# Kernel tuning notes

Measured on AMD Instinct MI355X. Metric: run time of the kernel, lower is better.

The kernel has to match this reference:

```python
import jax, jax.numpy as jnp
import numpy as np

B, T, D = 4, 4096, 1024
H, KP = 16, 256  # heads, low-rank seq projection dim
DK = D // H


def setup_inputs() -> dict:
    key = jax.random.key(0)
    ks = jax.random.split(key, 8)
    s = 1.0 / np.sqrt(D)
    xav = np.sqrt(6.0 / (T + KP))  # xavier_uniform for (max_seq_len, k_proj_dim)
    return {
        "x": jax.random.normal(ks[0], (B, T, D), jnp.float32),
        "Wq": jax.random.normal(ks[1], (D, D), jnp.float32) * s,
        "Wk": jax.random.normal(ks[2], (D, D), jnp.float32) * s,
        "Wv": jax.random.normal(ks[3], (D, D), jnp.float32) * s,
        "Ek": jax.random.uniform(ks[4], (T, KP), jnp.float32, -xav, xav),
        "Ev": jax.random.uniform(ks[5], (T, KP), jnp.float32, -xav, xav),
        "Wo": jax.random.normal(ks[6], (D, D), jnp.float32) * s,
        "bo": jnp.zeros((D,), jnp.float32),
    }


def reference(x, Wq, Wk, Wv, Ek, Ev, Wo, bo):
    Bx, Tx, _ = x.shape
    # QKV projections -> (B, H, T, DK)
    def split_heads(y):
        return y.reshape(Bx, Tx, H, DK).transpose(0, 2, 1, 3)
    Q = split_heads(x @ Wq)
    K = split_heads(x @ Wk)
    V = split_heads(x @ Wv)
    # Low-rank projection along sequence length: T -> KP
    K_proj = jnp.einsum('bhtd,tk->bhkd', K, Ek[:Tx])
    V_proj = jnp.einsum('bhtd,tk->bhkd', V, Ev[:Tx])
    scale = 1.0 / np.sqrt(DK)
    scores = jnp.einsum('bhtd,bhkd->bhtk', Q, K_proj) * scale
    attn = jax.nn.softmax(scores, axis=-1)
    ctx = jnp.einsum('bhtk,bhkd->bhtd', attn, V_proj)
    out = ctx.transpose(0, 2, 1, 3).reshape(Bx, Tx, D)
    return out @ Wo + bo  # dropout p=0.0 (eval) -> identity
```

## Files before the change

### kernel.cpp

```cpp
#include <hip/hip_runtime.h>

typedef unsigned short u16;
typedef __attribute__((ext_vector_type(8))) short short8;
typedef __attribute__((ext_vector_type(4))) float f32x4;

#define T_SEQ 4096
#define DMODEL 1024
#define NH 16
#define DKH 64
#define KPROJ 256

__device__ __forceinline__ u16 f2bf(float f) {
  union { float f; unsigned u; } v; v.f = f;
  unsigned r = v.u + 0x7FFFu + ((v.u >> 16) & 1u);
  return (u16)(r >> 16);
}
__device__ __forceinline__ float bf2f(u16 h) {
  union { unsigned u; float f; } v; v.u = ((unsigned)h) << 16; return v.f;
}
__device__ __forceinline__ unsigned cvt_pk_bf16(float a, float b) {
  unsigned r;
  asm("v_cvt_pk_bf16_f32 %0, %1, %2" : "=v"(r) : "v"(a), "v"(b));
  return r;
}

__device__ __forceinline__ void gl2lds16(const u16* g, u16* l) {
  __builtin_amdgcn_global_load_lds(
      (const __attribute__((address_space(1))) unsigned int*)g,
      (__attribute__((address_space(3))) unsigned int*)(unsigned int)(unsigned long long)l,
      16, 0, 0);
}

__global__ void sniff_dtype(const u16* __restrict__ x, int* __restrict__ flag) {
  int c = 0;
  for (int i = threadIdx.x; i < 8192; i += 64)
    if ((x[2 * i] & 0x7F80) == 0x7F80) c++;
#pragma unroll
  for (int m = 1; m < 64; m <<= 1) c += __shfl_xor(c, m);
  if (threadIdx.x == 0) *flag = (c > 0) ? 1 : 0;
}

__global__ void transpose_x(const void* __restrict__ in, u16* __restrict__ outT,
                            u16* __restrict__ outR, const int* __restrict__ flag) {
  __shared__ u16 tile[32][33];
  const bool f32 = (*flag != 0);
  const size_t zoff = (size_t)blockIdx.z * T_SEQ * DMODEL;
  const int c0 = blockIdx.x * 32, r0 = blockIdx.y * 32;
  for (int i = threadIdx.y; i < 32; i += 8) {
    const size_t idx = zoff + (size_t)(r0 + i) * DMODEL + c0 + threadIdx.x;
    const u16 v = f32 ? f2bf(((const float*)in)[idx]) : ((const u16*)in)[idx];
    tile[i][threadIdx.x] = v;
    outR[idx] = v;
  }
  __syncthreads();
  for (int i = threadIdx.y; i < 32; i += 8)
    outT[zoff + (size_t)(c0 + i) * T_SEQ + r0 + threadIdx.x] = tile[threadIdx.x][i];
}

__global__ void transpose_cvt4(const void* __restrict__ p0, const void* __restrict__ p1,
                               const void* __restrict__ p2, const void* __restrict__ p3,
                               u16* __restrict__ out, int R, int C, const int* __restrict__ flag) {
  __shared__ u16 tile[32][33];
  const bool f32 = (*flag != 0);
  const int z = blockIdx.z;
  const void* in = (z == 0) ? p0 : (z == 1) ? p1 : (z == 2) ? p2 : p3;
  const size_t zoff = (size_t)z * R * C;
  const int c0 = blockIdx.x * 32, r0 = blockIdx.y * 32;
  for (int i = threadIdx.y; i < 32; i += 8) {
    const size_t idx = (size_t)(r0 + i) * C + c0 + threadIdx.x;
    tile[i][threadIdx.x] = f32 ? f2bf(((const float*)in)[idx]) : ((const u16*)in)[idx];
  }
  __syncthreads();
  for (int i = threadIdx.y; i < 32; i += 8)
    out[zoff + (size_t)(c0 + i) * R + r0 + threadIdx.x] = tile[threadIdx.x][i];
}

__global__ void reduce_splitk(const float* __restrict__ P, u16* __restrict__ out) {
  const int b = blockIdx.y;
  const int j = (blockIdx.x * 256 + threadIdx.x) * 8;
  const float* p = P + (size_t)b * 4 * 524288 + j;
  float acc[8] = {};
#pragma unroll
  for (int s = 0; s < 4; ++s) {
    const float4 v0 = *(const float4*)(p + (size_t)s * 524288);
    const float4 v1 = *(const float4*)(p + (size_t)s * 524288 + 4);
    acc[0] += v0.x; acc[1] += v0.y; acc[2] += v0.z; acc[3] += v0.w;
    acc[4] += v1.x; acc[5] += v1.y; acc[6] += v1.z; acc[7] += v1.w;
  }
  union { u16 s[8]; short8 v; } o;
#pragma unroll
  for (int k = 0; k < 8; ++k) o.s[k] = f2bf(acc[k]);
  *(short8*)(out + (size_t)b * 524288 + j) = o.v;
}

template <int MODE>
__global__ void __launch_bounds__(256) gemm_bt(const u16* __restrict__ A0, const u16* __restrict__ Bt0,
                                               const void* __restrict__ bias, void* __restrict__ Cv,
                                               const int* __restrict__ flag, int M, int N, int K,
                                               int ldA, int ldB, size_t sA, size_t sB, size_t sC) {
  __shared__ __align__(16) u16 As[2][128 * 32];
  __shared__ __align__(16) u16 Bs[2][128 * 32];

  const int gx = gridDim.x, gy = gridDim.y;
  const int gxy = gx * gy;
  const int nwg = gxy * gridDim.z;
  int lin = (blockIdx.z * gy + blockIdx.y) * gx + blockIdx.x;
  if ((nwg & 7) == 0) lin = (lin & 7) * (nwg >> 3) + (lin >> 3);
  const int bz = lin / gxy;
  const int rem = lin - bz * gxy;
  const int by = rem / gx;
  const int bx = rem - by * gx;

  const int z = bz;
  const int bb = (MODE == 2) ? (z >> 2) : z;
  const int kstart = (MODE == 2) ? ((z & 3) * K) : 0;
  const u16* A = A0 + (size_t)bb * sA;
  const u16* Bt = Bt0 + (size_t)bb * sB;
  const int tid = threadIdx.x;
  const int wid = tid >> 6, lane = tid & 63;
  const int wm = wid >> 1, wn = wid & 1;
  const int quad = lane >> 4, l16 = lane & 15;
  const int m0 = by * 128, n0 = bx * 128;
  const int srow = lane >> 2, scol = (lane & 3) * 8;

  const u16* Ag = A + (size_t)(m0 + srow) * ldA + scol + kstart;
  const u16* Bg = Bt + (size_t)(n0 + srow) * ldB + scol + kstart;

  f32x4 acc[4][4] = {};

  auto stage = [&](int buf, int k0) {
#pragma unroll
    for (int r = 0; r < 2; ++r) {
      const int rowb = r * 64 + wid * 16;
      gl2lds16(Ag + (size_t)rowb * ldA + k0, &As[buf][rowb * 32]);
      gl2lds16(Bg + (size_t)rowb * ldB + k0, &Bs[buf][rowb * 32]);
    }
  };

  const int nI = K >> 5;
  stage(0, 0);
  __syncthreads();
  int cur = 0;

  for (int t = 0; t < nI; ++t) {
    if (t + 1 < nI) stage(cur ^ 1, (t + 1) << 5);
    short8 a[4], b[4];
#pragma unroll
    for (int mi = 0; mi < 4; ++mi)
      a[mi] = *(const short8*)(&As[cur][(wm * 64 + mi * 16 + l16) * 32 + quad * 8]);
#pragma unroll
    for (int ni = 0; ni < 4; ++ni)
      b[ni] = *(const short8*)(&Bs[cur][(wn * 64 + ni * 16 + l16) * 32 + quad * 8]);
#pragma unroll
    for (int mi = 0; mi < 4; ++mi)
#pragma unroll
      for (int ni = 0; ni < 4; ++ni)
        acc[mi][ni] = __builtin_amdgcn_mfma_f32_16x16x32_bf16(a[mi], b[ni], acc[mi][ni], 0, 0, 0);
    __syncthreads();
    cur ^= 1;
  }

  const bool f32out = (MODE == 1) && (*flag != 0);
  float* Pz = (MODE == 2) ? ((float*)Cv + (size_t)z * M * N) : nullptr;
#pragma unroll
  for (int mi = 0; mi < 4; ++mi) {
#pragma unroll
    for (int ni = 0; ni < 4; ++ni) {
      const int mloc = wm * 64 + mi * 16 + quad * 4;
      const int n = n0 + wn * 64 + ni * 16 + l16;
      float badd = 0.0f;
      if (MODE == 1)
        badd = f32out ? ((const float*)bias)[n] : bf2f(((const u16*)bias)[n]);
#pragma unroll
      for (int r = 0; r < 4; ++r) {
        if (MODE == 2) {
          Pz[(size_t)(m0 + mloc + r) * N + n] = acc[mi][ni][r];
        } else {
          const size_t oi = (size_t)bb * sC + (size_t)(m0 + mloc + r) * N + n;
          if (f32out) ((float*)Cv)[oi] = acc[mi][ni][r] + badd;
          else        ((u16*)Cv)[oi]  = f2bf(acc[mi][ni][r] + badd);
        }
      }
    }
  }
}

__global__ void __launch_bounds__(64, 2) attn_fused(const u16* Q, const u16* __restrict__ Kp,
                                                    const u16* __restrict__ VpT, u16* Ctx) {
  __shared__ __align__(16) u16 Ps[32 * 264];
  __shared__ __align__(16) float invS[32];
  int lin = blockIdx.y * gridDim.x + blockIdx.x;
  lin = (lin & 7) * ((gridDim.x * gridDim.y) >> 3) + (lin >> 3);
  const int bx = lin & 127;
  const int bh = lin >> 7;
  const int b = bh >> 4, h = bh & 15;
  const int t0 = bx * 32;
  const int lane = threadIdx.x;
  const int quad = lane >> 4, l16 = lane & 15;
  const u16* Qb = Q + ((size_t)b * T_SEQ + t0) * DMODEL + h * DKH;
  const u16* Kpb = Kp + (size_t)b * (KPROJ * DMODEL) + h * DKH;
  const u16* Vpb = VpT + (size_t)b * (DMODEL * KPROJ) + (size_t)(h * DKH) * KPROJ;

  short8 q[2][2];
#pragma unroll
  for (int kk = 0; kk < 2; ++kk) {
    q[kk][0] = *(const short8*)(Qb + (size_t)l16 * DMODEL + kk * 32 + quad * 8);
    q[kk][1] = *(const short8*)(Qb + (size_t)(16 + l16) * DMODEL + kk * 32 + quad * 8);
  }

  f32x4 s[16][2] = {};
  short8 kbuf[2][4];
#pragma unroll
  for (int i = 0; i < 4; ++i)
    kbuf[0][i] = *(const short8*)(Kpb + (size_t)(i * 16 + l16) * DMODEL + quad * 8);
#pragma unroll
  for (int ph = 0; ph < 8; ++ph) {
    const int cb = ph & 1, nb = cb ^ 1;
    if (ph < 7) {
      const int np = ph + 1, nkk = np >> 2, nq4 = np & 3;
#pragma unroll
      for (int i = 0; i < 4; ++i)
        kbuf[nb][i] = *(const short8*)(Kpb + (size_t)((nq4 * 4 + i) * 16 + l16) * DMODEL +
                                       nkk * 32 + quad * 8);
    }
    const int kk = ph >> 2, q4 = ph & 3;
    __builtin_amdgcn_s_setprio(1);
#pragma unroll
    for (int i = 0; i < 4; ++i) {
      s[q4 * 4 + i][0] =
          __builtin_amdgcn_mfma_f32_16x16x32_bf16(kbuf[cb][i], q[kk][0], s[q4 * 4 + i][0], 0, 0, 0);
      s[q4 * 4 + i][1] =
          __builtin_amdgcn_mfma_f32_16x16x32_bf16(kbuf[cb][i], q[kk][1], s[q4 * 4 + i][1], 0, 0, 0);
    }
    __builtin_amdgcn_s_setprio(0);
  }

  short8 vbuf[2][4];
#pragma unroll
  for (int ni = 0; ni < 4; ++ni)
    vbuf[0][ni] = *(const short8*)(Vpb + (size_t)(ni * 16 + l16) * KPROJ + quad * 8);

  const float sc = 0.125f * 1.44269504f;
  float sm0 = 0.0f, sm1 = 0.0f;
#pragma unroll
  for (int mi = 0; mi < 16; ++mi) {
    const float a0 = exp2f(s[mi][0][0] * sc);
    const float a1 = exp2f(s[mi][0][1] * sc);
    const float a2 = exp2f(s[mi][0][2] * sc);
    const float a3 = exp2f(s[mi][0][3] * sc);
    const float b0 = exp2f(s[mi][1][0] * sc);
    const float b1 = exp2f(s[mi][1][1] * sc);
    const float b2 = exp2f(s[mi][1][2] * sc);
    const float b3 = exp2f(s[mi][1][3] * sc);
    sm0 += (a0 + a1) + (a2 + a3);
    sm1 += (b0 + b1) + (b2 + b3);
    *(uint2*)(Ps + l16 * 264 + mi * 16 + quad * 4) =
        make_uint2(cvt_pk_bf16(a0, a1), cvt_pk_bf16(a2, a3));
    *(uint2*)(Ps + (16 + l16) * 264 + mi * 16 + quad * 4) =
        make_uint2(cvt_pk_bf16(b0, b1), cvt_pk_bf16(b2, b3));
  }
  sm0 += __shfl_xor(sm0, 16); sm0 += __shfl_xor(sm0, 32);
  sm1 += __shfl_xor(sm1, 16); sm1 += __shfl_xor(sm1, 32);
  if (quad == 0) {
    invS[l16] = 1.0f / sm0;
    invS[16 + l16] = 1.0f / sm1;
  }

  f32x4 c0[4] = {}, c1[4] = {};
#pragma unroll
  for (int kki = 0; kki < 8; ++kki) {
    const int cb = kki & 1, nb = cb ^ 1;
    if (kki < 7) {
#pragma unroll
      for (int ni = 0; ni < 4; ++ni)
        vbuf[nb][ni] = *(const short8*)(Vpb + (size_t)(ni * 16 + l16) * KPROJ +
                                        (kki + 1) * 32 + quad * 8);
    }
    short8 a0 = *(const short8*)(Ps + (size_t)l16 * 264 + kki * 32 + quad * 8);
    short8 a1 = *(const short8*)(Ps + (size_t)(16 + l16) * 264 + kki * 32 + quad * 8);
    __builtin_amdgcn_s_setprio(1);
#pragma unroll
    for (int ni = 0; ni < 4; ++ni) {
      c0[ni] = __builtin_amdgcn_mfma_f32_16x16x32_bf16(a0, vbuf[cb][ni], c0[ni], 0, 0, 0);
      c1[ni] = __builtin_amdgcn_mfma_f32_16x16x32_bf16(a1, vbuf[cb][ni], c1[ni], 0, 0, 0);
    }
    __builtin_amdgcn_s_setprio(0);
  }

  const float4 iv0 = *(const float4*)(invS + quad * 4);
  const float4 iv1 = *(const float4*)(invS + 16 + quad * 4);
  const float ivr0[4] = {iv0.x, iv0.y, iv0.z, iv0.w};
  const float ivr1[4] = {iv1.x, iv1.y, iv1.z, iv1.w};
#pragma unroll
  for (int ni = 0; ni < 4; ++ni)
#pragma unroll
    for (int r = 0; r < 4; ++r) {
      Ctx[((size_t)b * T_SEQ + t0 + quad * 4 + r) * DMODEL + h * DKH + ni * 16 + l16] =
          f2bf(c0[ni][r] * ivr0[r]);
      Ctx[((size_t)b * T_SEQ + t0 + 16 + quad * 4 + r) * DMODEL + h * DKH + ni * 16 + l16] =
          f2bf(c1[ni][r] * ivr1[r]);
    }
}

extern "C" void kernel_launch(void* const* d_in, const int* in_sizes, int n_in,
                              void* d_out, int out_size, void* d_ws, size_t ws_size,
                              hipStream_t stream) {
  (void)in_sizes; (void)n_in; (void)out_size; (void)ws_size;

  int* flag = (int*)d_ws;
  u16* base = (u16*)d_ws + 16;
  const size_t WSZ = 1048576;
  const size_t XSZ = 16777216;
  u16* wqT   = base + 0 * WSZ;
  u16* wkT   = base + 1 * WSZ;
  u16* wvT   = base + 2 * WSZ;
  u16* woT   = base + 3 * WSZ;
  u16* ekevT = base + 4 * WSZ;
  u16* xT    = base + 6 * WSZ;
  u16* xE    = xT + XSZ;
  u16* Kp    = xE + 4 * 524288;
  u16* VpT   = Kp + 4 * 262144;
  u16* Q     = VpT + 4 * 262144;
  u16* xbf   = (u16*)d_out;
  float* xEp = (float*)Q;

  sniff_dtype<<<1, 64, 0, stream>>>((const u16*)d_in[0], flag);

  dim3 tb(32, 8);
  transpose_x<<<dim3(32, 128, 4), tb, 0, stream>>>(d_in[0], xT, xbf, flag);
  transpose_cvt4<<<dim3(32, 32, 4), tb, 0, stream>>>(d_in[1], d_in[2], d_in[3], d_in[6],
                                                     wqT, 1024, 1024, flag);
  transpose_cvt4<<<dim3(8, 128, 2), tb, 0, stream>>>(d_in[4], d_in[5], nullptr, nullptr,
                                                     ekevT, 4096, 256, flag);

  gemm_bt<2><<<dim3(8, 4, 16), 256, 0, stream>>>(ekevT, xT, nullptr, xEp, flag,
                                                 512, 1024, 1024, 4096, 4096,
                                                 0, (size_t)DMODEL * T_SEQ, 0);
  reduce_splitk<<<dim3(256, 4), 256, 0, stream>>>(xEp, xE);

  gemm_bt<0><<<dim3(8, 2, 4), 256, 0, stream>>>(xE, wkT, nullptr, Kp, flag,
                                                256, 1024, 1024, 1024, 1024, 524288, 0, 262144);
  gemm_bt<0><<<dim3(2, 8, 4), 256, 0, stream>>>(wvT, xE + 262144, nullptr, VpT, flag,
                                                1024, 256, 1024, 1024, 1024, 0, 524288, 262144);
  gemm_bt<0><<<dim3(8, 128, 1), 256, 0, stream>>>(xbf, wqT, nullptr, Q, flag,
                                                  16384, 1024, 1024, 1024, 1024, 0, 0, 0);

  attn_fused<<<dim3(128, 64), 64, 0, stream>>>(Q, Kp, VpT, Q );

  gemm_bt<1><<<dim3(8, 128, 1), 256, 0, stream>>>(Q, woT, d_in[7], d_out, flag,
                                                  16384, 1024, 1024, 1024, 1024, 0, 0, 0);
}
```

Measured before the change: 472.1 us.

## Interleave QK, exp and PV per 32-key tile in attention kernel

```diff
diff --git a/kernel.cpp b/kernel.cpp
--- a/kernel.cpp
+++ b/kernel.cpp
@@ -185,9 +185,52 @@
   }
 }
 
-__global__ void __launch_bounds__(64, 2) attn_fused(const u16* Q, const u16* __restrict__ Kp,
+#define ATTN_TILE(KT, KC, KN, VC, VN, DO_PRE)                                                \
+  {                                                                                          \
+    if (DO_PRE) {                                                                            \
+      _Pragma("unroll") for (int m = 0; m < 2; ++m)                                          \
+        _Pragma("unroll") for (int k2 = 0; k2 < 2; ++k2)                                     \
+          KN[m][k2] = *(const short8*)(Kpb + (size_t)((((KT) + 1) * 2 + m) * 16 + l16) * DMODEL + \
+                                       k2 * 32 + quad * 8);                                  \
+      _Pragma("unroll") for (int ni = 0; ni < 4; ++ni)                                       \
+        VN[ni] = *(const short8*)(Vpb + (size_t)(ni * 16 + l16) * KPROJ + ((KT) + 1) * 32 +  \
+                                  quad * 8);                                                 \
+    }                                                                                        \
+    f32x4 st[2][2] = {};                                                                     \
+    __builtin_amdgcn_s_setprio(1);                                                          \
+    _Pragma("unroll") for (int m = 0; m < 2; ++m)                                            \
+      _Pragma("unroll") for (int k2 = 0; k2 < 2; ++k2) {                                     \
+        st[m][0] = __builtin_amdgcn_mfma_f32_16x16x32_bf16(KC[m][k2], q[k2][0], st[m][0], 0, 0, 0); \
+        st[m][1] = __builtin_amdgcn_mfma_f32_16x16x32_bf16(KC[m][k2], q[k2][1], st[m][1], 0, 0, 0); \
+      }                                                                                      \
+    __builtin_amdgcn_s_setprio(0);                                                          \
+    _Pragma("unroll") for (int m = 0; m < 2; ++m) {                                          \
+      const float a0 = exp2f(st[m][0][0] * sc), a1 = exp2f(st[m][0][1] * sc);                \
+      const float a2 = exp2f(st[m][0][2] * sc), a3 = exp2f(st[m][0][3] * sc);                \
+      const float b0 = exp2f(st[m][1][0] * sc), b1 = exp2f(st[m][1][1] * sc);                \
+      const float b2 = exp2f(st[m][1][2] * sc), b3 = exp2f(st[m][1][3] * sc);                \
+      sm0 += (a0 + a1) + (a2 + a3);                                                          \
+      sm1 += (b0 + b1) + (b2 + b3);                                                          \
+      *(uint2*)(Ps + (l16) * 36 + m * 16 + quad * 4) =                                       \
+          make_uint2(cvt_pk_bf16(a0, a1), cvt_pk_bf16(a2, a3));                              \
+      *(uint2*)(Ps + (16 + l16) * 36 + m * 16 + quad * 4) =                                  \
+          make_uint2(cvt_pk_bf16(b0, b1), cvt_pk_bf16(b2, b3));                              \
+    }                                                                                        \
+    {                                                                                        \
+      short8 pa0 = *(const short8*)(Ps + (size_t)l16 * 36 + quad * 8);                       \
+      short8 pa1 = *(const short8*)(Ps + (size_t)(16 + l16) * 36 + quad * 8);                \
+      __builtin_amdgcn_s_setprio(1);                                                        \
+      _Pragma("unroll") for (int ni = 0; ni < 4; ++ni) {                                     \
+        c0[ni] = __builtin_amdgcn_mfma_f32_16x16x32_bf16(pa0, VC[ni], c0[ni], 0, 0, 0);      \
+        c1[ni] = __builtin_amdgcn_mfma_f32_16x16x32_bf16(pa1, VC[ni], c1[ni], 0, 0, 0);      \
+      }                                                                                      \
+      __builtin_amdgcn_s_setprio(0);                                                        \
+    }                                                                                        \
+  }
+
+__global__ void __launch_bounds__(64, 3) attn_fused(const u16* Q, const u16* __restrict__ Kp,
                                                     const u16* __restrict__ VpT, u16* Ctx) {
-  __shared__ __align__(16) u16 Ps[32 * 264];
+  __shared__ __align__(16) u16 Ps[32 * 36];
   __shared__ __align__(16) float invS[32];
   int lin = blockIdx.y * gridDim.x + blockIdx.x;
   lin = (lin & 7) * ((gridDim.x * gridDim.y) >> 3) + (lin >> 3);
@@ -208,83 +251,34 @@
     q[kk][1] = *(const short8*)(Qb + (size_t)(16 + l16) * DMODEL + kk * 32 + quad * 8);
   }
 
-  f32x4 s[16][2] = {};
-  short8 kbuf[2][4];
-#pragma unroll
-  for (int i = 0; i < 4; ++i)
-    kbuf[0][i] = *(const short8*)(Kpb + (size_t)(i * 16 + l16) * DMODEL + quad * 8);
-#pragma unroll
-  for (int ph = 0; ph < 8; ++ph) {
-    const int cb = ph & 1, nb = cb ^ 1;
-    if (ph < 7) {
-      const int np = ph + 1, nkk = np >> 2, nq4 = np & 3;
-#pragma unroll
-      for (int i = 0; i < 4; ++i)
-        kbuf[nb][i] = *(const short8*)(Kpb + (size_t)((nq4 * 4 + i) * 16 + l16) * DMODEL +
-                                       nkk * 32 + quad * 8);
-    }
-    const int kk = ph >> 2, q4 = ph & 3;
-    __builtin_amdgcn_s_setprio(1);
-#pragma unroll
-    for (int i = 0; i < 4; ++i) {
-      s[q4 * 4 + i][0] =
-          __builtin_amdgcn_mfma_f32_16x16x32_bf16(kbuf[cb][i], q[kk][0], s[q4 * 4 + i][0], 0, 0, 0);
-      s[q4 * 4 + i][1] =
-          __builtin_amdgcn_mfma_f32_16x16x32_bf16(kbuf[cb][i], q[kk][1], s[q4 * 4 + i][1], 0, 0, 0);
-    }
-    __builtin_amdgcn_s_setprio(0);
-  }
-
-  short8 vbuf[2][4];
+  short8 kA[2][2], kB[2][2], vA[4], vB[4];
+#pragma unroll
+  for (int m = 0; m < 2; ++m)
+#pragma unroll
+    for (int k2 = 0; k2 < 2; ++k2)
+      kA[m][k2] = *(const short8*)(Kpb + (size_t)((m)*16 + l16) * DMODEL + k2 * 32 + quad * 8);
 #pragma unroll
   for (int ni = 0; ni < 4; ++ni)
-    vbuf[0][ni] = *(const short8*)(Vpb + (size_t)(ni * 16 + l16) * KPROJ + quad * 8);
-
+    vA[ni] = *(const short8*)(Vpb + (size_t)(ni * 16 + l16) * KPROJ + quad * 8);
+
+  f32x4 c0[4] = {}, c1[4] = {};
+  float sm0 = 0.0f, sm1 = 0.0f;
   const float sc = 0.125f * 1.44269504f;
-  float sm0 = 0.0f, sm1 = 0.0f;
-#pragma unroll
-  for (int mi = 0; mi < 16; ++mi) {
-    const float a0 = exp2f(s[mi][0][0] * sc);
-    const float a1 = exp2f(s[mi][0][1] * sc);
-    const float a2 = exp2f(s[mi][0][2] * sc);
-    const float a3 = exp2f(s[mi][0][3] * sc);
-    const float b0 = exp2f(s[mi][1][0] * sc);
-    const float b1 = exp2f(s[mi][1][1] * sc);
-    const float b2 = exp2f(s[mi][1][2] * sc);
-    const float b3 = exp2f(s[mi][1][3] * sc);
-    sm0 += (a0 + a1) + (a2 + a3);
-    sm1 += (b0 + b1) + (b2 + b3);
-    *(uint2*)(Ps + l16 * 264 + mi * 16 + quad * 4) =
-        make_uint2(cvt_pk_bf16(a0, a1), cvt_pk_bf16(a2, a3));
-    *(uint2*)(Ps + (16 + l16) * 264 + mi * 16 + quad * 4) =
-        make_uint2(cvt_pk_bf16(b0, b1), cvt_pk_bf16(b2, b3));
-  }
+
+  ATTN_TILE(0, kA, kB, vA, vB, 1)
+  ATTN_TILE(1, kB, kA, vB, vA, 1)
+  ATTN_TILE(2, kA, kB, vA, vB, 1)
+  ATTN_TILE(3, kB, kA, vB, vA, 1)
+  ATTN_TILE(4, kA, kB, vA, vB, 1)
+  ATTN_TILE(5, kB, kA, vB, vA, 1)
+  ATTN_TILE(6, kA, kB, vA, vB, 1)
+  ATTN_TILE(7, kB, kA, vB, vA, 0)
+
   sm0 += __shfl_xor(sm0, 16); sm0 += __shfl_xor(sm0, 32);
   sm1 += __shfl_xor(sm1, 16); sm1 += __shfl_xor(sm1, 32);
   if (quad == 0) {
     invS[l16] = 1.0f / sm0;
     invS[16 + l16] = 1.0f / sm1;
-  }
-
-  f32x4 c0[4] = {}, c1[4] = {};
-#pragma unroll
-  for (int kki = 0; kki < 8; ++kki) {
-    const int cb = kki & 1, nb = cb ^ 1;
-    if (kki < 7) {
-#pragma unroll
-      for (int ni = 0; ni < 4; ++ni)
-        vbuf[nb][ni] = *(const short8*)(Vpb + (size_t)(ni * 16 + l16) * KPROJ +
-                                        (kki + 1) * 32 + quad * 8);
-    }
-    short8 a0 = *(const short8*)(Ps + (size_t)l16 * 264 + kki * 32 + quad * 8);
-    short8 a1 = *(const short8*)(Ps + (size_t)(16 + l16) * 264 + kki * 32 + quad * 8);
-    __builtin_amdgcn_s_setprio(1);
-#pragma unroll
-    for (int ni = 0; ni < 4; ++ni) {
-      c0[ni] = __builtin_amdgcn_mfma_f32_16x16x32_bf16(a0, vbuf[cb][ni], c0[ni], 0, 0, 0);
-      c1[ni] = __builtin_amdgcn_mfma_f32_16x16x32_bf16(a1, vbuf[cb][ni], c1[ni], 0, 0, 0);
-    }
-    __builtin_amdgcn_s_setprio(0);
   }
 
   const float4 iv0 = *(const float4*)(invS + quad * 4);
```

Measured after the change: 471.7 us. No clear change (-0.1%).

## Stage per-head K/V projections in LDS shared by four waves and fuse softmax-PV per tile

Applied to the files above, without the earlier changes.

```diff
diff --git a/kernel.cpp b/kernel.cpp
--- a/kernel.cpp
+++ b/kernel.cpp
@@ -185,21 +185,44 @@
   }
 }
 
-__global__ void __launch_bounds__(64, 2) attn_fused(const u16* Q, const u16* __restrict__ Kp,
-                                                    const u16* __restrict__ VpT, u16* Ctx) {
-  __shared__ __align__(16) u16 Ps[32 * 264];
-  __shared__ __align__(16) float invS[32];
+__global__ void __launch_bounds__(256, 2) attn_fused(const u16* Q, const u16* __restrict__ Kp,
+                                                     const u16* __restrict__ VpT, u16* Ctx) {
+  __shared__ __align__(16) u16 Ks[KPROJ * DKH];
+  __shared__ __align__(16) u16 Vs[DKH * KPROJ];
+  __shared__ __align__(16) u16 Ps[4 * 32 * 36];
+  __shared__ __align__(16) float invS[4 * 32];
+
   int lin = blockIdx.y * gridDim.x + blockIdx.x;
-  lin = (lin & 7) * ((gridDim.x * gridDim.y) >> 3) + (lin >> 3);
-  const int bx = lin & 127;
-  const int bh = lin >> 7;
+  lin = (lin & 7) * 256 + (lin >> 3);
+  const int bx = lin & 31;
+  const int bh = lin >> 5;
   const int b = bh >> 4, h = bh & 15;
-  const int t0 = bx * 32;
-  const int lane = threadIdx.x;
+  const int tid = threadIdx.x, wid = tid >> 6, lane = tid & 63;
   const int quad = lane >> 4, l16 = lane & 15;
+  const int t0 = bx * 128 + wid * 32;
   const u16* Qb = Q + ((size_t)b * T_SEQ + t0) * DMODEL + h * DKH;
   const u16* Kpb = Kp + (size_t)b * (KPROJ * DMODEL) + h * DKH;
   const u16* Vpb = VpT + (size_t)b * (DMODEL * KPROJ) + (size_t)(h * DKH) * KPROJ;
+  u16* PsW = Ps + wid * (32 * 36);
+  float* invW = invS + wid * 32;
+
+  {
+    const int srow = lane >> 3;
+    const int scolb = ((lane & 7) * 16) ^ ((srow & 7) << 4);
+#pragma unroll
+    for (int i = 0; i < 8; ++i) {
+      const int rbase = wid * 64 + i * 8;
+      gl2lds16(Kpb + (size_t)(rbase + srow) * DMODEL + (scolb >> 1), Ks + rbase * DKH);
+    }
+    const int vrow = lane >> 5;
+#pragma unroll
+    for (int j = 0; j < 8; ++j) {
+      const int dbase = wid * 16 + j * 2;
+      const int d = dbase + vrow;
+      const int vcolb = ((lane & 31) * 16) ^ ((d & 7) << 4);
+      gl2lds16(Vpb + (size_t)d * KPROJ + (vcolb >> 1), Vs + dbase * KPROJ);
+    }
+  }
 
   short8 q[2][2];
 #pragma unroll
@@ -208,87 +231,75 @@
     q[kk][1] = *(const short8*)(Qb + (size_t)(16 + l16) * DMODEL + kk * 32 + quad * 8);
   }
 
-  f32x4 s[16][2] = {};
-  short8 kbuf[2][4];
-#pragma unroll
-  for (int i = 0; i < 4; ++i)
-    kbuf[0][i] = *(const short8*)(Kpb + (size_t)(i * 16 + l16) * DMODEL + quad * 8);
-#pragma unroll
-  for (int ph = 0; ph < 8; ++ph) {
-    const int cb = ph & 1, nb = cb ^ 1;
-    if (ph < 7) {
-      const int np = ph + 1, nkk = np >> 2, nq4 = np & 3;
-#pragma unroll
-      for (int i = 0; i < 4; ++i)
-        kbuf[nb][i] = *(const short8*)(Kpb + (size_t)((nq4 * 4 + i) * 16 + l16) * DMODEL +
-                                       nkk * 32 + quad * 8);
-    }
-    const int kk = ph >> 2, q4 = ph & 3;
+  __syncthreads();
+
+  f32x4 c0[4] = {}, c1[4] = {};
+  float sm0 = 0.0f, sm1 = 0.0f;
+  const float sc = 0.125f * 1.44269504f;
+
+#pragma unroll
+  for (int kt = 0; kt < 8; ++kt) {
+    short8 kf[2][2];
+#pragma unroll
+    for (int m = 0; m < 2; ++m)
+#pragma unroll
+      for (int k2 = 0; k2 < 2; ++k2) {
+        const int row = kt * 32 + m * 16 + l16;
+        const int off = ((k2 * 64 + quad * 16) ^ ((row & 7) << 4)) >> 1;
+        kf[m][k2] = *(const short8*)(Ks + row * DKH + off);
+      }
+    f32x4 st[2][2] = {};
     __builtin_amdgcn_s_setprio(1);
 #pragma unroll
-    for (int i = 0; i < 4; ++i) {
-      s[q4 * 4 + i][0] =
-          __builtin_amdgcn_mfma_f32_16x16x32_bf16(kbuf[cb][i], q[kk][0], s[q4 * 4 + i][0], 0, 0, 0);
-      s[q4 * 4 + i][1] =
-          __builtin_amdgcn_mfma_f32_16x16x32_bf16(kbuf[cb][i], q[kk][1], s[q4 * 4 + i][1], 0, 0, 0);
-    }
+    for (int m = 0; m < 2; ++m)
+#pragma unroll
+      for (int k2 = 0; k2 < 2; ++k2) {
+        st[m][0] = __builtin_amdgcn_mfma_f32_16x16x32_bf16(kf[m][k2], q[k2][0], st[m][0], 0, 0, 0);
+        st[m][1] = __builtin_amdgcn_mfma_f32_16x16x32_bf16(kf[m][k2], q[k2][1], st[m][1], 0, 0, 0);
+      }
     __builtin_amdgcn_s_setprio(0);
-  }
-
-  short8 vbuf[2][4];
-#pragma unroll
-  for (int ni = 0; ni < 4; ++ni)
-    vbuf[0][ni] = *(const short8*)(Vpb + (size_t)(ni * 16 + l16) * KPROJ + quad * 8);
-
-  const float sc = 0.125f * 1.44269504f;
-  float sm0 = 0.0f, sm1 = 0.0f;
-#pragma unroll
-  for (int mi = 0; mi < 16; ++mi) {
-    const float a0 = exp2f(s[mi][0][0] * sc);
-    const float a1 = exp2f(s[mi][0][1] * sc);
-    const float a2 = exp2f(s[mi][0][2] * sc);
-    const float a3 = exp2f(s[mi][0][3] * sc);
-    const float b0 = exp2f(s[mi][1][0] * sc);
-    const float b1 = exp2f(s[mi][1][1] * sc);
-    const float b2 = exp2f(s[mi][1][2] * sc);
-    const float b3 = exp2f(s[mi][1][3] * sc);
-    sm0 += (a0 + a1) + (a2 + a3);
-    sm1 += (b0 + b1) + (b2 + b3);
-    *(uint2*)(Ps + l16 * 264 + mi * 16 + quad * 4) =
-        make_uint2(cvt_pk_bf16(a0, a1), cvt_pk_bf16(a2, a3));
-    *(uint2*)(Ps + (16 + l16) * 264 + mi * 16 + quad * 4) =
-        make_uint2(cvt_pk_bf16(b0, b1), cvt_pk_bf16(b2, b3));
-  }
+
+#pragma unroll
+    for (int m = 0; m < 2; ++m) {
+      const float a0 = exp2f(st[m][0][0] * sc), a1 = exp2f(st[m][0][1] * sc);
+      const float a2 = exp2f(st[m][0][2] * sc), a3 = exp2f(st[m][0][3] * sc);
+      const float b0 = exp2f(st[m][1][0] * sc), b1 = exp2f(st[m][1][1] * sc);
+      const float b2 = exp2f(st[m][1][2] * sc), b3 = exp2f(st[m][1][3] * sc);
+      sm0 += (a0 + a1) + (a2 + a3);
+      sm1 += (b0 + b1) + (b2 + b3);
+      *(uint2*)(PsW + l16 * 36 + m * 16 + quad * 4) =
+          make_uint2(cvt_pk_bf16(a0, a1), cvt_pk_bf16(a2, a3));
+      *(uint2*)(PsW + (16 + l16) * 36 + m * 16 + quad * 4) =
+          make_uint2(cvt_pk_bf16(b0, b1), cvt_pk_bf16(b2, b3));
+    }
+
+    short8 vf[4];
+#pragma unroll
+    for (int ni = 0; ni < 4; ++ni) {
+      const int d = ni * 16 + l16;
+      const int off = ((kt * 64 + quad * 16) ^ ((d & 7) << 4)) >> 1;
+      vf[ni] = *(const short8*)(Vs + d * KPROJ + off);
+    }
+    short8 pa0 = *(const short8*)(PsW + (size_t)l16 * 36 + quad * 8);
+    short8 pa1 = *(const short8*)(PsW + (size_t)(16 + l16) * 36 + quad * 8);
+    __builtin_amdgcn_s_setprio(1);
+#pragma unroll
+    for (int ni = 0; ni < 4; ++ni) {
+      c0[ni] = __builtin_amdgcn_mfma_f32_16x16x32_bf16(pa0, vf[ni], c0[ni], 0, 0, 0);
+      c1[ni] = __builtin_amdgcn_mfma_f32_16x16x32_bf16(pa1, vf[ni], c1[ni], 0, 0, 0);
+    }
+    __builtin_amdgcn_s_setprio(0);
+  }
+
   sm0 += __shfl_xor(sm0, 16); sm0 += __shfl_xor(sm0, 32);
   sm1 += __shfl_xor(sm1, 16); sm1 += __shfl_xor(sm1, 32);
   if (quad == 0) {
-    invS[l16] = 1.0f / sm0;
-    invS[16 + l16] = 1.0f / sm1;
-  }
-
-  f32x4 c0[4] = {}, c1[4] = {};
-#pragma unroll
-  for (int kki = 0; kki < 8; ++kki) {
-    const int cb = kki & 1, nb = cb ^ 1;
-    if (kki < 7) {
-#pragma unroll
-      for (int ni = 0; ni < 4; ++ni)
-        vbuf[nb][ni] = *(const short8*)(Vpb + (size_t)(ni * 16 + l16) * KPROJ +
-                                        (kki + 1) * 32 + quad * 8);
-    }
-    short8 a0 = *(const short8*)(Ps + (size_t)l16 * 264 + kki * 32 + quad * 8);
-    short8 a1 = *(const short8*)(Ps + (size_t)(16 + l16) * 264 + kki * 32 + quad * 8);
-    __builtin_amdgcn_s_setprio(1);
-#pragma unroll
-    for (int ni = 0; ni < 4; ++ni) {
-      c0[ni] = __builtin_amdgcn_mfma_f32_16x16x32_bf16(a0, vbuf[cb][ni], c0[ni], 0, 0, 0);
-      c1[ni] = __builtin_amdgcn_mfma_f32_16x16x32_bf16(a1, vbuf[cb][ni], c1[ni], 0, 0, 0);
-    }
-    __builtin_amdgcn_s_setprio(0);
-  }
-
-  const float4 iv0 = *(const float4*)(invS + quad * 4);
-  const float4 iv1 = *(const float4*)(invS + 16 + quad * 4);
+    invW[l16] = 1.0f / sm0;
+    invW[16 + l16] = 1.0f / sm1;
+  }
+
+  const float4 iv0 = *(const float4*)(invW + quad * 4);
+  const float4 iv1 = *(const float4*)(invW + 16 + quad * 4);
   const float ivr0[4] = {iv0.x, iv0.y, iv0.z, iv0.w};
   const float ivr1[4] = {iv1.x, iv1.y, iv1.z, iv1.w};
 #pragma unroll
@@ -345,7 +356,7 @@
   gemm_bt<0><<<dim3(8, 128, 1), 256, 0, stream>>>(xbf, wqT, nullptr, Q, flag,
                                                   16384, 1024, 1024, 1024, 1024, 0, 0, 0);
 
-  attn_fused<<<dim3(128, 64), 64, 0, stream>>>(Q, Kp, VpT, Q );
+  attn_fused<<<dim3(32, 64), 256, 0, stream>>>(Q, Kp, VpT, Q );
 
   gemm_bt<1><<<dim3(8, 128, 1), 256, 0, stream>>>(Q, woT, d_in[7], d_out, flag,
                                                   16384, 1024, 1024, 1024, 1024, 0, 0, 0);
```

Result: faster. 444.1 us (-5.9%).
